# Performance work log

Hardware: AMD Instinct MI355X
Metric: run time of the kernel (lower is better)

Reference implementation:

```python
import jax, jax.numpy as jnp
import numpy as np

RES = 64
C_DIM = 64
N_BLOCKS = 4
EPS = 1e-12


def conv2d(x, w, b, pad):
    out = jax.lax.conv_general_dilated(
        x, w, window_strides=(1, 1), padding=[(pad, pad), (pad, pad)],
        dimension_numbers=('NCHW', 'OIHW', 'NCHW'))
    return out + b[None, :, None, None]


def unfold3(x):
    # F.unfold(kernel=3, padding=1): [B,C,H,W] -> [B, C*9, H*W], torch ordering (c, ki, kj)
    B, C, H, W = x.shape
    xp = jnp.pad(x, ((0, 0), (0, 0), (1, 1), (1, 1)))
    patches = jnp.stack([xp[:, :, ki:ki + H, kj:kj + W]
                         for ki in range(3) for kj in range(3)], axis=2)  # [B,C,9,H,W]
    return patches.reshape(B, C * 9, H * W)


def fold3(t, H, W):
    # F.fold(kernel=3, padding=1): sum overlapping patches back to [B,C,H,W]
    B, C9, L = t.shape
    C = C9 // 9
    t = t.reshape(B, C, 3, 3, H, W)
    out = jnp.zeros((B, C, H + 2, W + 2), t.dtype)
    for ki in range(3):
        for kj in range(3):
            out = out.at[:, :, ki:ki + H, kj:kj + W].add(t[:, :, ki, kj])
    return out[:, :, 1:H + 1, 1:W + 1]


def setup_inputs() -> dict:
    key = jax.random.key(0)
    ks = jax.random.split(key, 16)
    B, L, C = 4, RES * RES, C_DIM
    s = 0.05
    inp = {
        'c0': jax.random.normal(ks[0], (B, L, C), jnp.float32),
        'f0': jax.random.normal(ks[1], (B, L, C), jnp.float32),
        'c1': jax.random.normal(ks[2], (B, L, C), jnp.float32),
        'head_w': jax.random.normal(ks[3], (C, C, 5, 5), jnp.float32) * s,
        'head_b': jax.random.normal(ks[4], (C,), jnp.float32) * s,
        'rb_w1': jax.random.normal(ks[5], (N_BLOCKS, C, C, 3, 3), jnp.float32) * s,
        'rb_b1': jax.random.normal(ks[6], (N_BLOCKS, C), jnp.float32) * s,
        'rb_w2': jax.random.normal(ks[7], (N_BLOCKS, C, C, 3, 3), jnp.float32) * s,
        'rb_b2': jax.random.normal(ks[8], (N_BLOCKS, C), jnp.float32) * s,
        'tail_w': jax.random.normal(ks[9], (C, C, 5, 5), jnp.float32) * s,
        'tail_b': jax.random.normal(ks[10], (C,), jnp.float32) * s,
        'sq_w': jax.random.normal(ks[11], (C, 2 * C, 5, 5), jnp.float32) * s,
        'sq_b': jax.random.normal(ks[12], (C,), jnp.float32) * s,
    }
    return inp


def reference(c0, f0, c1, head_w, head_b, rb_w1, rb_b1, rb_w2, rb_b2,
              tail_w, tail_b, sq_w, sq_b):
    B, L, C = c1.shape
    H = W = RES
    c1 = c1.swapaxes(1, 2).reshape(B, C, H, W)
    c0 = c0.swapaxes(1, 2).reshape(B, C, H, W)
    f0 = f0.swapaxes(1, 2).reshape(B, C, H, W)
    Delta_c = c1 - c0

    # --- search_Trans: patch correlation + best-match texture transfer ---
    c1u = unfold3(c1)                       # [B, C9, L]
    c0u = unfold3(c0).swapaxes(1, 2)        # [B, L, C9]
    c0n = c0u / jnp.maximum(jnp.linalg.norm(c0u, axis=2, keepdims=True), EPS)
    c1n = c1u / jnp.maximum(jnp.linalg.norm(c1u, axis=1, keepdims=True), EPS)
    R = jnp.einsum('blk,bkm->blm', c0n, c1n)  # [B, L, L]
    R_star = jnp.max(R, axis=1)               # [B, L]
    R_arg = jnp.argmax(R, axis=1)              # [B, L]
    f0u = unfold3(f0)                          # [B, C9, L]
    Tu = jnp.take_along_axis(f0u, R_arg[:, None, :], axis=2)
    T = fold3(Tu, H, W) / 9.0                  # [B, C, H, W]
    S = R_star.reshape(B, 1, H, W)

    # --- residual conv stack on Delta_c ---
    x1 = conv2d(Delta_c, head_w, head_b, 2)
    x = x1
    for i in range(rb_w1.shape[0]):  # NOTE: original feeds x1 into every block
        h = jax.nn.relu(conv2d(x1, rb_w1[i], rb_b1[i], 1))
        x = conv2d(h, rb_w2[i], rb_b2[i], 1) + x1
    x = conv2d(x, tail_w, tail_b, 2)
    Delta_c_fea = x + x1

    x = conv2d(jnp.concatenate([Delta_c_fea, T], axis=1), sq_w, sq_b, 2)
    out = Delta_c_fea + x * S
    return out.reshape(B, C, L).swapaxes(1, 2)
```

## Files before the change

### kernel.cpp

```cpp
#include <hip/hip_runtime.h>
#include <hip/hip_bf16.h>


#define BATCH 4

typedef unsigned short u16;
typedef unsigned int   u32;
typedef __attribute__((ext_vector_type(8))) short short8;
typedef __attribute__((ext_vector_type(4))) float f32x4;

__device__ __forceinline__ void bsplit2(float a, float b, u32& ho, u32& lo) {
  __hip_bfloat16 ha = __float2bfloat16(a), hb = __float2bfloat16(b);
  float ra = a - __bfloat162float(ha), rb = b - __bfloat162float(hb);
  __hip_bfloat16 la = __float2bfloat16(ra), lb = __float2bfloat16(rb);
  ho = (u32)*(u16*)&ha | ((u32)*(u16*)&hb << 16);
  lo = (u32)*(u16*)&la | ((u32)*(u16*)&lb << 16);
}

__device__ __forceinline__ void gload_lds16(const void* g, void* l) {
  __builtin_amdgcn_global_load_lds((const __attribute__((address_space(1))) void*)g,
                                   (__attribute__((address_space(3))) void*)l, 16, 0, 0);
}

__global__ __launch_bounds__(256) void prep_ss(const float* __restrict__ c0,
    const float* __restrict__ c1, float* __restrict__ ss0, float* __restrict__ ss1)
{
  int tid = blockIdx.x * 256 + threadIdx.x;
  const float* p0 = c0 + (size_t)tid * 64;
  const float* p1 = c1 + (size_t)tid * 64;
  float s0 = 0.f, s1 = 0.f;
  for (int c = 0; c < 64; ++c) {
    float a = p0[c]; s0 += a * a;
    float b = p1[c]; s1 += b * b;
  }
  ss0[tid] = s0;
  ss1[tid] = s1;
}

__global__ __launch_bounds__(256) void norm_kernel(const float* __restrict__ ss0,
    const float* __restrict__ ss1, float* __restrict__ inv0, float* __restrict__ inv1)
{
  int tid = blockIdx.x * 256 + threadIdx.x;
  int b = tid >> 12, l = tid & 4095;
  int y = l >> 6, x = l & 63;
  int base = b << 12;
  float s0 = 0.f, s1 = 0.f;
  for (int dy = -1; dy <= 1; ++dy) {
    int yy = y + dy; if (yy < 0 || yy >= 64) continue;
    for (int dx = -1; dx <= 1; ++dx) {
      int xx = x + dx; if (xx < 0 || xx >= 64) continue;
      int ii = base + (yy << 6) + xx;
      s0 += ss0[ii]; s1 += ss1[ii];
    }
  }
  inv0[tid] = 1.f / fmaxf(sqrtf(s0), 1e-12f);
  inv1[tid] = 1.f / fmaxf(sqrtf(s1), 1e-12f);
}

__global__ __launch_bounds__(256) void split_pad_kernel(const float* __restrict__ c0,
    const float* __restrict__ c1, u16* __restrict__ p0h, u16* __restrict__ p0l,
    u16* __restrict__ p1h, u16* __restrict__ p1l)
{
  int b = blockIdx.y, t = threadIdx.x;
  int pix = blockIdx.x * 4 + (t >> 6);
  int c = t & 63;
  int py = pix / 66, px = pix - py * 66;
  size_t d = ((size_t)b * 4356 + pix) * 64 + c;
  float v0 = 0.f, v1 = 0.f;
  if (py >= 1 && py <= 64 && px >= 1 && px <= 64) {
    size_t s = (((size_t)b << 12) + ((py - 1) << 6) + (px - 1)) * 64 + c;
    v0 = c0[s]; v1 = c1[s];
  }
  __hip_bfloat16 h = __float2bfloat16(v0);
  float r = v0 - __bfloat162float(h);
  __hip_bfloat16 lo = __float2bfloat16(r);
  p0h[d] = *(u16*)&h; p0l[d] = *(u16*)&lo;
  h = __float2bfloat16(v1);
  r = v1 - __bfloat162float(h);
  lo = __float2bfloat16(r);
  p1h[d] = *(u16*)&h; p1l[d] = *(u16*)&lo;
}

__global__ __launch_bounds__(256) void wprep(const float* __restrict__ src,
    u16* __restrict__ wh, u16* __restrict__ wl, int Cin, int KK, int n)
{
  int i = blockIdx.x * 256 + threadIdx.x;
  if (i >= n) return;
  int per = Cin * KK;
  int cout = i / per;
  int rem = i - cout * per;
  int cin = rem / KK;
  int tap = rem - cin * KK;
  float x = src[i];
  __hip_bfloat16 h = __float2bfloat16(x);
  float r = x - __bfloat162float(h);
  __hip_bfloat16 lo = __float2bfloat16(r);
  int d = (tap * 64 + cout) * Cin + cin;
  wh[d] = *(u16*)&h;
  wl[d] = *(u16*)&lo;
}

__global__ __launch_bounds__(256) void corr_mfma(const u16* __restrict__ p0h,
    const u16* __restrict__ p0l, const u16* __restrict__ p1h, const u16* __restrict__ p1l,
    const float* __restrict__ inv0, float* __restrict__ pval, int* __restrict__ pidx)
{
  __shared__ __align__(16) u16 smem[32768];
  int mt = blockIdx.x, lt = blockIdx.y, b = blockIdx.z;
  int t = threadIdx.x;
  int lane = t & 63, w = t >> 6;
  int wl = w >> 1, wm = w & 1;
  int cc = lane & 15, q = lane >> 4;
  const size_t boff = (size_t)b * 278784;
  const u16* msrc = (w == 0) ? p0h : (w == 1) ? p0l : (w == 2) ? p1h : p1l;
  msrc += boff;
  const float* inv0b = inv0 + (b << 12);
  int isB = w >> 1;

  int srow0 = lane >> 2;
  int cs_g  = (lane & 3) ^ ((lane >> 3) & 3);
  int sw    = (cc >> 1) & 3;

  auto stage = [&](int ssub, int sph, u16* dst) {
    int r = sph >> 1, hh = sph & 1;
    int ki = r / 3, kj = r - ki * 3;
    int pb = isB ? (mt << 7) : ((lt << 9) + (ssub << 7));
#pragma unroll
    for (int it = 0; it < 8; ++it) {
      int p = pb + (it << 4) + srow0;
      int ypad = (p >> 6) + ki, xpad = (p & 63) + kj;
      const u16* g = msrc + (((size_t)(ypad * 66 + xpad)) << 6) + (hh << 5) + (cs_g << 3);
      gload_lds16(g, dst + (it << 9));
    }
  };

  float bval[4] = {-1e30f, -1e30f, -1e30f, -1e30f};
  int   bidx[4] = {0, 0, 0, 0};

  stage(0, 0, smem + (w << 12));

  for (int sub = 0; sub < 4; ++sub) {
    int row0 = (lt << 9) + (sub << 7);
    f32x4 acc[4][4];
#pragma unroll
    for (int i = 0; i < 4; ++i)
#pragma unroll
      for (int j = 0; j < 4; ++j) acc[i][j] = (f32x4){0.f, 0.f, 0.f, 0.f};

    for (int ph = 0; ph < 18; ++ph) {
      int g = sub * 18 + ph;
      int nxt = g + 1;
      if (nxt < 72) {
        int np = ph + 1, ns = sub;
        if (np == 18) { np = 0; ++ns; }
        stage(ns, np, smem + ((nxt & 1) << 14) + (w << 12));
        asm volatile("s_waitcnt vmcnt(8)" ::: "memory");
      } else {
        asm volatile("s_waitcnt vmcnt(0)" ::: "memory");
      }
      __builtin_amdgcn_s_barrier();
      __builtin_amdgcn_sched_barrier(0);
      const u16* bb = smem + ((g & 1) << 14);
      short8 afh[4], afl[4], bfh[4], bfl[4];
#pragma unroll
      for (int i = 0; i < 4; ++i) {
        int ra = (((wl << 6) + (i << 4) + cc) << 5) + ((q ^ sw) << 3);
        afh[i] = *(const short8*)(&bb[ra]);
        afl[i] = *(const short8*)(&bb[4096 + ra]);
      }
#pragma unroll
      for (int j = 0; j < 4; ++j) {
        int rb = (((wm << 6) + (j << 4) + cc) << 5) + ((q ^ sw) << 3);
        bfh[j] = *(const short8*)(&bb[8192 + rb]);
        bfl[j] = *(const short8*)(&bb[12288 + rb]);
      }
#pragma unroll
      for (int i = 0; i < 4; ++i)
#pragma unroll
        for (int j = 0; j < 4; ++j) {
          acc[i][j] = __builtin_amdgcn_mfma_f32_16x16x32_bf16(afh[i], bfl[j], acc[i][j], 0, 0, 0);
          acc[i][j] = __builtin_amdgcn_mfma_f32_16x16x32_bf16(afl[i], bfh[j], acc[i][j], 0, 0, 0);
          acc[i][j] = __builtin_amdgcn_mfma_f32_16x16x32_bf16(afh[i], bfh[j], acc[i][j], 0, 0, 0);
        }
      __builtin_amdgcn_sched_barrier(0);
      __builtin_amdgcn_s_barrier();
    }
#pragma unroll
    for (int i = 0; i < 4; ++i) {
#pragma unroll
      for (int rg = 0; rg < 4; ++rg) {
        int l = row0 + (wl << 6) + (i << 4) + (q << 2) + rg;
        float sc = inv0b[l];
#pragma unroll
        for (int j = 0; j < 4; ++j) {
          float v = acc[i][j][rg] * sc;
          if (v > bval[j]) { bval[j] = v; bidx[j] = l; }
        }
      }
    }
  }

  __syncthreads();
  float* lval = (float*)smem;
  int*   lidx = (int*)((char*)smem + 4096);
  int slot = (wl << 2) + q;
#pragma unroll
  for (int j = 0; j < 4; ++j) {
    int col = (wm << 6) + (j << 4) + cc;
    lval[col * 8 + slot] = bval[j];
    lidx[col * 8 + slot] = bidx[j];
  }
  __syncthreads();
  if (t < 128) {
    float bv = -1e30f; int bi = 0x7FFFFFFF;
    for (int s = 0; s < 8; ++s) {
      float v = lval[t * 8 + s]; int id = lidx[t * 8 + s];
      if (v > bv || (v == bv && id < bi)) { bv = v; bi = id; }
    }
    size_t o = (size_t)(((b << 3) + lt) << 12) + (mt << 7) + t;
    pval[o] = bv; pidx[o] = bi;
  }
}

__global__ __launch_bounds__(256) void reduce_kernel(const float* __restrict__ pval,
    const int* __restrict__ pidx, const float* __restrict__ inv1,
    float* __restrict__ S, int* __restrict__ arg)
{
  int tid = blockIdx.x * 256 + threadIdx.x;
  int b = tid >> 12, m = tid & 4095;
  float bv = -1e30f; int bi = 0x7FFFFFFF;
  for (int lt = 0; lt < 8; ++lt) {
    size_t o = (size_t)(((b << 3) + lt) << 12) + m;
    float v = pval[o]; int id = pidx[o];
    if (v > bv || (v == bv && id < bi)) { bv = v; bi = id; }
  }
  S[tid] = bv * inv1[tid];
  arg[tid] = ((unsigned)bi < 4096u) ? bi : 0;
}

__global__ __launch_bounds__(256) void tgather_kernel(const float* __restrict__ f0,
    const int* __restrict__ arg, float* __restrict__ T)
{
  __shared__ int a3[192];
  int y = blockIdx.x, b = blockIdx.y, t = threadIdx.x;
  if (t < 192) {
    int r = t >> 6, xx = t & 63;
    int yy = y + r - 1;
    a3[t] = (yy >= 0 && yy < 64) ? arg[(b << 12) + (yy << 6) + xx] : 0;
  }
  __syncthreads();
  int c = t & 63, pg = t >> 6;
  for (int it = 0; it < 16; ++it) {
    int px = pg + (it << 2);
    float sum = 0.f;
#pragma unroll
    for (int ki = 0; ki < 3; ++ki) {
      int yn = y + 1 - ki;
      if (yn < 0 || yn >= 64) continue;
#pragma unroll
      for (int kj = 0; kj < 3; ++kj) {
        int xn = px + 1 - kj;
        if (xn < 0 || xn >= 64) continue;
        int p = a3[((2 - ki) << 6) + xn];
        int sy = (p >> 6) + ki - 1, sx = (p & 63) + kj - 1;
        if (sy >= 0 && sy < 64 && sx >= 0 && sx < 64)
          sum += f0[((((size_t)b << 12) + (sy << 6) + sx) << 6) + c];
      }
    }
    T[((((size_t)b << 12) + (y << 6) + px)) * 64 + c] = sum * (1.f / 9.f);
  }
}

template<int KS, int CINCH>
__global__ __launch_bounds__(256) void conv_mfma(const float* __restrict__ in0,
    const float* __restrict__ in1, const u16* __restrict__ whp, const u16* __restrict__ wlp,
    const float* __restrict__ bias, float* __restrict__ outp,
    const float* __restrict__ res, int dorelu, int dm)
{
  constexpr int P = KS / 2;
  constexpr int CIN = CINCH * 32;
  __shared__ __align__(16) u16 Ah[32 * 40], Al[32 * 40];
  __shared__ __align__(16) u16 Bh[64 * 40], Bl[64 * 40];
  int tile = blockIdx.x, b = blockIdx.y;
  int t = threadIdx.x;
  int lane = t & 63, w = t >> 6;
  int wpx = w >> 1, wm = w & 1;
  int cc = lane & 15, q = lane >> 4;
  int ty = tile >> 1, txb = (tile & 1) << 5;
  const size_t abase = (size_t)b << 12;
  f32x4 acc[2];
#pragma unroll
  for (int j = 0; j < 2; ++j) acc[j] = (f32x4){0.f, 0.f, 0.f, 0.f};

  for (int tap = 0; tap < KS * KS; ++tap) {
    int ki = tap / KS, kj = tap - ki * KS;
    int iy = ty + ki - P;
    for (int kk = 0; kk < CINCH; ++kk) {
      __syncthreads();
      if (t < 128) {
        int row = t >> 2, cs = t & 3;
        int ix = txb + row + kj - P;
        float v[8];
#pragma unroll
        for (int e = 0; e < 8; ++e) v[e] = 0.f;
        if ((unsigned)iy < 64u && (unsigned)ix < 64u) {
          size_t base = (abase + (iy << 6) + ix) << 6;
          int cg = kk * 32 + (cs << 3);
          if (dm) {
            float4 a0 = *(const float4*)(in0 + base + cg);
            float4 a1 = *(const float4*)(in0 + base + cg + 4);
            float4 b0 = *(const float4*)(in1 + base + cg);
            float4 b1 = *(const float4*)(in1 + base + cg + 4);
            v[0] = b0.x - a0.x; v[1] = b0.y - a0.y; v[2] = b0.z - a0.z; v[3] = b0.w - a0.w;
            v[4] = b1.x - a1.x; v[5] = b1.y - a1.y; v[6] = b1.z - a1.z; v[7] = b1.w - a1.w;
          } else {
            const float* sp = (CINCH == 4 && cg >= 64) ? (in1 + base + (cg - 64))
                                                       : (in0 + base + cg);
            float4 a0 = *(const float4*)sp;
            float4 a1 = *(const float4*)(sp + 4);
            v[0] = a0.x; v[1] = a0.y; v[2] = a0.z; v[3] = a0.w;
            v[4] = a1.x; v[5] = a1.y; v[6] = a1.z; v[7] = a1.w;
          }
        }
        uint4 uh, ul;
        bsplit2(v[0], v[1], uh.x, ul.x);
        bsplit2(v[2], v[3], uh.y, ul.y);
        bsplit2(v[4], v[5], uh.z, ul.z);
        bsplit2(v[6], v[7], uh.w, ul.w);
        *(uint4*)&Ah[row * 40 + (cs << 3)] = uh;
        *(uint4*)&Al[row * 40 + (cs << 3)] = ul;
      } else {
        int tb = t - 128;
#pragma unroll
        for (int rr = 0; rr < 2; ++rr) {
          int idx = tb * 2 + rr;
          int cout = idx >> 2, cs = idx & 3;
          size_t so = (size_t)(tap * 64 + cout) * CIN + kk * 32 + (cs << 3);
          uint4 vh = *(const uint4*)&whp[so];
          uint4 vl = *(const uint4*)&wlp[so];
          *(uint4*)&Bh[cout * 40 + (cs << 3)] = vh;
          *(uint4*)&Bl[cout * 40 + (cs << 3)] = vl;
        }
      }
      __syncthreads();
      short8 afh, afl, bfh[2], bfl[2];
      {
        int ra = ((wpx << 4) + cc) * 40 + (q << 3);
        afh = *(const short8*)&Ah[ra];
        afl = *(const short8*)&Al[ra];
      }
#pragma unroll
      for (int j = 0; j < 2; ++j) {
        int rb = ((wm << 5) + (j << 4) + cc) * 40 + (q << 3);
        bfh[j] = *(const short8*)&Bh[rb];
        bfl[j] = *(const short8*)&Bl[rb];
      }
#pragma unroll
      for (int j = 0; j < 2; ++j) {
        acc[j] = __builtin_amdgcn_mfma_f32_16x16x32_bf16(afh, bfl[j], acc[j], 0, 0, 0);
        acc[j] = __builtin_amdgcn_mfma_f32_16x16x32_bf16(afl, bfh[j], acc[j], 0, 0, 0);
        acc[j] = __builtin_amdgcn_mfma_f32_16x16x32_bf16(afh, bfh[j], acc[j], 0, 0, 0);
      }
    }
  }
#pragma unroll
  for (int rg = 0; rg < 4; ++rg) {
    int p = (ty << 6) + txb + (wpx << 4) + (q << 2) + rg;
#pragma unroll
    for (int j = 0; j < 2; ++j) {
      int cout = (wm << 5) + (j << 4) + cc;
      float v = acc[j][rg] + bias[cout];
      if (dorelu) v = fmaxf(v, 0.f);
      size_t oi = ((abase + p) << 6) + cout;
      if (res) v += res[oi];
      outp[oi] = v;
    }
  }
}

__global__ __launch_bounds__(256) void final_kernel(const float* __restrict__ dcf,
    const float* __restrict__ xs, const float* __restrict__ S, float* __restrict__ out)
{
  int tid = blockIdx.x * 256 + threadIdx.x;
  out[tid] = dcf[tid] + xs[tid] * S[tid >> 6];
}

extern "C" void kernel_launch(void* const* d_in, const int* in_sizes, int n_in,
                              void* d_out, int out_size, void* d_ws, size_t ws_size,
                              hipStream_t stream)
{
  (void)in_sizes; (void)n_in; (void)out_size; (void)ws_size;
  const float* c0     = (const float*)d_in[0];
  const float* f0     = (const float*)d_in[1];
  const float* c1     = (const float*)d_in[2];
  const float* head_w = (const float*)d_in[3];
  const float* head_b = (const float*)d_in[4];
  const float* rb_w1  = (const float*)d_in[5];
  const float* rb_b1  = (const float*)d_in[6];
  const float* rb_w2  = (const float*)d_in[7];
  const float* rb_b2  = (const float*)d_in[8];
  const float* tail_w = (const float*)d_in[9];
  const float* tail_b = (const float*)d_in[10];
  const float* sq_w   = (const float*)d_in[11];
  const float* sq_b   = (const float*)d_in[12];
  float* out = (float*)d_out;
  char* ws = (char*)d_ws;

  const size_t OFF_SS0  = 0;
  const size_t OFF_SS1  = 65536;
  const size_t OFF_INV0 = 131072;
  const size_t OFF_INV1 = 196608;
  const size_t OFF_S    = 262144;
  const size_t OFF_ARG  = 327680;
  const size_t OFF_PVAL = 393216;
  const size_t OFF_PIDX = 917504;
  const size_t OFF_WHH  = 1441792;
  const size_t OFF_WHL  = 1646592;
  const size_t OFF_W1H  = 1851392;
  const size_t OFF_W1L  = 1925120;
  const size_t OFF_W2H  = 1998848;
  const size_t OFF_W2L  = 2072576;
  const size_t OFF_WTH  = 2146304;
  const size_t OFF_WTL  = 2351104;
  const size_t OFF_WSH  = 2555904;
  const size_t OFF_WSL  = 2965504;
  const size_t OFF_P0H  = 3375104;
  const size_t OFF_P0L  = OFF_P0H + 2230272;
  const size_t OFF_P1H  = OFF_P0L + 2230272;
  const size_t OFF_P1L  = OFF_P1H + 2230272;
  const size_t OFF_SA   = 3375104;
  const size_t OFF_SB   = 7569408;
  const size_t OFF_SC   = 11763712;

  float* ss0  = (float*)(ws + OFF_SS0);
  float* ss1  = (float*)(ws + OFF_SS1);
  float* inv0 = (float*)(ws + OFF_INV0);
  float* inv1 = (float*)(ws + OFF_INV1);
  float* Sbuf = (float*)(ws + OFF_S);
  int*   argb = (int*)(ws + OFF_ARG);
  float* pval = (float*)(ws + OFF_PVAL);
  int*   pidx = (int*)(ws + OFF_PIDX);
  u16* whh = (u16*)(ws + OFF_WHH); u16* whl = (u16*)(ws + OFF_WHL);
  u16* w1h = (u16*)(ws + OFF_W1H); u16* w1l = (u16*)(ws + OFF_W1L);
  u16* w2h = (u16*)(ws + OFF_W2H); u16* w2l = (u16*)(ws + OFF_W2L);
  u16* wth = (u16*)(ws + OFF_WTH); u16* wtl = (u16*)(ws + OFF_WTL);
  u16* wsh = (u16*)(ws + OFF_WSH); u16* wsl = (u16*)(ws + OFF_WSL);
  u16* p0h = (u16*)(ws + OFF_P0H); u16* p0l = (u16*)(ws + OFF_P0L);
  u16* p1h = (u16*)(ws + OFF_P1H); u16* p1l = (u16*)(ws + OFF_P1L);
  float* x1  = (float*)(ws + OFF_SA);
  float* Tb  = (float*)(ws + OFF_SA);
  float* hb  = (float*)(ws + OFF_SB);
  float* dcf = (float*)(ws + OFF_SB);
  float* xb  = (float*)(ws + OFF_SC);
  float* xsb = (float*)(ws + OFF_SC);

  dim3 b256(256);
  prep_ss<<<dim3(64), b256, 0, stream>>>(c0, c1, ss0, ss1);
  norm_kernel<<<dim3(64), b256, 0, stream>>>(ss0, ss1, inv0, inv1);
  split_pad_kernel<<<dim3(1089, BATCH), b256, 0, stream>>>(c0, c1, p0h, p0l, p1h, p1l);
  wprep<<<dim3(400), b256, 0, stream>>>(head_w, whh, whl, 64, 25, 102400);
  wprep<<<dim3(144), b256, 0, stream>>>(rb_w1 + 110592, w1h, w1l, 64, 9, 36864);
  wprep<<<dim3(144), b256, 0, stream>>>(rb_w2 + 110592, w2h, w2l, 64, 9, 36864);
  wprep<<<dim3(400), b256, 0, stream>>>(tail_w, wth, wtl, 64, 25, 102400);
  wprep<<<dim3(800), b256, 0, stream>>>(sq_w, wsh, wsl, 128, 25, 204800);

  corr_mfma<<<dim3(32, 8, BATCH), b256, 0, stream>>>(p0h, p0l, p1h, p1l, inv0, pval, pidx);
  reduce_kernel<<<dim3(64), b256, 0, stream>>>(pval, pidx, inv1, Sbuf, argb);

  dim3 cgrid(128, BATCH);
  conv_mfma<5, 2><<<cgrid, b256, 0, stream>>>(c0, c1, whh, whl, head_b, x1, nullptr, 0, 1);
  conv_mfma<3, 2><<<cgrid, b256, 0, stream>>>(x1, nullptr, w1h, w1l, rb_b1 + 192, hb, nullptr, 1, 0);
  conv_mfma<3, 2><<<cgrid, b256, 0, stream>>>(hb, nullptr, w2h, w2l, rb_b2 + 192, xb, x1, 0, 0);
  conv_mfma<5, 2><<<cgrid, b256, 0, stream>>>(xb, nullptr, wth, wtl, tail_b, dcf, x1, 0, 0);

  tgather_kernel<<<dim3(64, BATCH), b256, 0, stream>>>(f0, argb, Tb);
  conv_mfma<5, 4><<<cgrid, b256, 0, stream>>>(dcf, Tb, wsh, wsl, sq_b, xsb, nullptr, 0, 0);

  final_kernel<<<dim3(4096), b256, 0, stream>>>(dcf, xsb, Sbuf, out);
}
```

Measured before the change: 555.3 us.

## Double-buffer LDS tiles and prefetch next slice into registers in conv_mfma

Restructures the conv_mfma main loop into a flat iteration over tap×channel-chunk with two LDS buffers. Global loads for the next iteration are issued into registers before the current MFMA work, then split and written to the alternate buffer, so only one barrier per iteration remains. The aim is to hide global load latency behind MFMA and cut synchronisation. The cost is doubled LDS use and extra registers, which may lower occupancy. The single barrier relies on a hand-placed waitcnt and s_barrier being enough to order reads of one buffer against writes to the other.

```diff
diff --git a/kernel.cpp b/kernel.cpp
--- a/kernel.cpp
+++ b/kernel.cpp
@@ -278,8 +278,10 @@
 {
   constexpr int P = KS / 2;
   constexpr int CIN = CINCH * 32;
-  __shared__ __align__(16) u16 Ah[32 * 40], Al[32 * 40];
-  __shared__ __align__(16) u16 Bh[64 * 40], Bl[64 * 40];
+  constexpr int KSH = (CINCH == 2) ? 1 : 2;
+  constexpr int NIT = KS * KS * CINCH;
+  __shared__ __align__(16) u16 Ah[2][32 * 40], Al[2][32 * 40];
+  __shared__ __align__(16) u16 Bh[2][64 * 40], Bl[2][64 * 40];
   int tile = blockIdx.x, b = blockIdx.y;
   int t = threadIdx.x;
   int lane = t & 63, w = t >> 6;
@@ -288,87 +290,115 @@
   int ty = tile >> 1, txb = (tile & 1) << 5;
   const size_t abase = (size_t)b << 12;
   f32x4 acc[2];
-#pragma unroll
-  for (int j = 0; j < 2; ++j) acc[j] = (f32x4){0.f, 0.f, 0.f, 0.f};
-
-  for (int tap = 0; tap < KS * KS; ++tap) {
-    int ki = tap / KS, kj = tap - ki * KS;
-    int iy = ty + ki - P;
-    for (int kk = 0; kk < CINCH; ++kk) {
-      __syncthreads();
-      if (t < 128) {
-        int row = t >> 2, cs = t & 3;
-        int ix = txb + row + kj - P;
-        float v[8];
-#pragma unroll
-        for (int e = 0; e < 8; ++e) v[e] = 0.f;
-        if ((unsigned)iy < 64u && (unsigned)ix < 64u) {
-          size_t base = (abase + (iy << 6) + ix) << 6;
-          int cg = kk * 32 + (cs << 3);
-          if (dm) {
-            float4 a0 = *(const float4*)(in0 + base + cg);
-            float4 a1 = *(const float4*)(in0 + base + cg + 4);
-            float4 b0 = *(const float4*)(in1 + base + cg);
-            float4 b1 = *(const float4*)(in1 + base + cg + 4);
-            v[0] = b0.x - a0.x; v[1] = b0.y - a0.y; v[2] = b0.z - a0.z; v[3] = b0.w - a0.w;
-            v[4] = b1.x - a1.x; v[5] = b1.y - a1.y; v[6] = b1.z - a1.z; v[7] = b1.w - a1.w;
-          } else {
-            const float* sp = (CINCH == 4 && cg >= 64) ? (in1 + base + (cg - 64))
-                                                       : (in0 + base + cg);
-            float4 a0 = *(const float4*)sp;
-            float4 a1 = *(const float4*)(sp + 4);
-            v[0] = a0.x; v[1] = a0.y; v[2] = a0.z; v[3] = a0.w;
-            v[4] = a1.x; v[5] = a1.y; v[6] = a1.z; v[7] = a1.w;
-          }
+  acc[0] = (f32x4){0.f, 0.f, 0.f, 0.f};
+  acc[1] = (f32x4){0.f, 0.f, 0.f, 0.f};
+
+  uint4 rg[4];
+  int arow = t >> 2, acs = t & 3;
+  int tb = t - 128;
+
+  auto issue_loads = [&](int itn) {
+    int tapn = itn >> KSH, kkn = itn & (CINCH - 1);
+    int ki = tapn / KS, kj = tapn - ki * KS;
+    if (t < 128) {
+      rg[0] = rg[1] = rg[2] = rg[3] = make_uint4(0u, 0u, 0u, 0u);
+      int iy = ty + ki - P;
+      int ix = txb + arow + kj - P;
+      if ((unsigned)iy < 64u && (unsigned)ix < 64u) {
+        size_t base = (abase + (iy << 6) + ix) << 6;
+        int cg = kkn * 32 + (acs << 3);
+        if (dm) {
+          rg[0] = *(const uint4*)(in0 + base + cg);
+          rg[1] = *(const uint4*)(in0 + base + cg + 4);
+          rg[2] = *(const uint4*)(in1 + base + cg);
+          rg[3] = *(const uint4*)(in1 + base + cg + 4);
+        } else {
+          const float* sp = (CINCH == 4 && cg >= 64) ? (in1 + base + (cg - 64))
+                                                     : (in0 + base + cg);
+          rg[0] = *(const uint4*)sp;
+          rg[1] = *(const uint4*)(sp + 4);
         }
-        uint4 uh, ul;
-        bsplit2(v[0], v[1], uh.x, ul.x);
-        bsplit2(v[2], v[3], uh.y, ul.y);
-        bsplit2(v[4], v[5], uh.z, ul.z);
-        bsplit2(v[6], v[7], uh.w, ul.w);
-        *(uint4*)&Ah[row * 40 + (cs << 3)] = uh;
-        *(uint4*)&Al[row * 40 + (cs << 3)] = ul;
+      }
+    } else {
+#pragma unroll
+      for (int rr = 0; rr < 2; ++rr) {
+        int idx = tb * 2 + rr;
+        int cout = idx >> 2, cs = idx & 3;
+        size_t so = (size_t)(tapn * 64 + cout) * CIN + kkn * 32 + (cs << 3);
+        rg[rr]     = *(const uint4*)&whp[so];
+        rg[2 + rr] = *(const uint4*)&wlp[so];
+      }
+    }
+  };
+
+  auto write_lds = [&](int cur) {
+    if (t < 128) {
+      float v[8];
+      if (dm) {
+#pragma unroll
+        for (int e = 0; e < 4; ++e) {
+          v[e]     = __uint_as_float((&rg[2].x)[e]) - __uint_as_float((&rg[0].x)[e]);
+          v[4 + e] = __uint_as_float((&rg[3].x)[e]) - __uint_as_float((&rg[1].x)[e]);
+        }
       } else {
-        int tb = t - 128;
-#pragma unroll
-        for (int rr = 0; rr < 2; ++rr) {
-          int idx = tb * 2 + rr;
-          int cout = idx >> 2, cs = idx & 3;
-          size_t so = (size_t)(tap * 64 + cout) * CIN + kk * 32 + (cs << 3);
-          uint4 vh = *(const uint4*)&whp[so];
-          uint4 vl = *(const uint4*)&wlp[so];
-          *(uint4*)&Bh[cout * 40 + (cs << 3)] = vh;
-          *(uint4*)&Bl[cout * 40 + (cs << 3)] = vl;
+#pragma unroll
+        for (int e = 0; e < 4; ++e) {
+          v[e]     = __uint_as_float((&rg[0].x)[e]);
+          v[4 + e] = __uint_as_float((&rg[1].x)[e]);
         }
       }
-      __syncthreads();
-      short8 afh, afl, bfh[2], bfl[2];
-      {
-        int ra = ((wpx << 4) + cc) * 40 + (q << 3);
-        afh = *(const short8*)&Ah[ra];
-        afl = *(const short8*)&Al[ra];
-      }
-#pragma unroll
-      for (int j = 0; j < 2; ++j) {
-        int rb = ((wm << 5) + (j << 4) + cc) * 40 + (q << 3);
-        bfh[j] = *(const short8*)&Bh[rb];
-        bfl[j] = *(const short8*)&Bl[rb];
-      }
-#pragma unroll
-      for (int j = 0; j < 2; ++j) {
-        acc[j] = __builtin_amdgcn_mfma_f32_16x16x32_bf16(afh, bfl[j], acc[j], 0, 0, 0);
-        acc[j] = __builtin_amdgcn_mfma_f32_16x16x32_bf16(afl, bfh[j], acc[j], 0, 0, 0);
-        acc[j] = __builtin_amdgcn_mfma_f32_16x16x32_bf16(afh, bfh[j], acc[j], 0, 0, 0);
-      }
-    }
-  }
-#pragma unroll
-  for (int rg = 0; rg < 4; ++rg) {
-    int p = (ty << 6) + txb + (wpx << 4) + (q << 2) + rg;
+      uint4 uh, ul;
+      bsplit2(v[0], v[1], uh.x, ul.x);
+      bsplit2(v[2], v[3], uh.y, ul.y);
+      bsplit2(v[4], v[5], uh.z, ul.z);
+      bsplit2(v[6], v[7], uh.w, ul.w);
+      *(uint4*)&Ah[cur][arow * 40 + (acs << 3)] = uh;
+      *(uint4*)&Al[cur][arow * 40 + (acs << 3)] = ul;
+    } else {
+#pragma unroll
+      for (int rr = 0; rr < 2; ++rr) {
+        int idx = tb * 2 + rr;
+        int cout = idx >> 2, cs = idx & 3;
+        *(uint4*)&Bh[cur][cout * 40 + (cs << 3)] = rg[rr];
+        *(uint4*)&Bl[cur][cout * 40 + (cs << 3)] = rg[2 + rr];
+      }
+    }
+  };
+
+  issue_loads(0);
+  for (int it = 0; it < NIT; ++it) {
+    int cur = it & 1;
+    write_lds(cur);
+    if (it + 1 < NIT) issue_loads(it + 1);
+    asm volatile("s_waitcnt lgkmcnt(0)" ::: "memory");
+    __builtin_amdgcn_s_barrier();
+    __builtin_amdgcn_sched_barrier(0);
+    short8 afh, afl, bfh[2], bfl[2];
+    {
+      int ra = ((wpx << 4) + cc) * 40 + (q << 3);
+      afh = *(const short8*)&Ah[cur][ra];
+      afl = *(const short8*)&Al[cur][ra];
+    }
+#pragma unroll
+    for (int j = 0; j < 2; ++j) {
+      int rb = ((wm << 5) + (j << 4) + cc) * 40 + (q << 3);
+      bfh[j] = *(const short8*)&Bh[cur][rb];
+      bfl[j] = *(const short8*)&Bl[cur][rb];
+    }
+#pragma unroll
+    for (int j = 0; j < 2; ++j) {
+      acc[j] = __builtin_amdgcn_mfma_f32_16x16x32_bf16(afh, bfl[j], acc[j], 0, 0, 0);
+      acc[j] = __builtin_amdgcn_mfma_f32_16x16x32_bf16(afl, bfh[j], acc[j], 0, 0, 0);
+      acc[j] = __builtin_amdgcn_mfma_f32_16x16x32_bf16(afh, bfh[j], acc[j], 0, 0, 0);
+    }
+  }
+#pragma unroll
+  for (int rgi = 0; rgi < 4; ++rgi) {
+    int p = (ty << 6) + txb + (wpx << 4) + (q << 2) + rgi;
 #pragma unroll
     for (int j = 0; j < 2; ++j) {
       int cout = (wm << 5) + (j << 4) + cc;
-      float v = acc[j][rg] + bias[cout];
+      float v = acc[j][rgi] + bias[cout];
       if (dorelu) v = fmaxf(v, 0.f);
       size_t oi = ((abase + p) << 6) + cout;
       if (res) v += res[oi];
```

Measured after the change: 529.4 us. 4.7% less time.
